# Performance work log

Measured on AMD Instinct MI355X. Metric: run time of the kernel, lower is better.

The kernel has to match this reference:

```python
import jax, jax.numpy as jnp
import numpy as np

N_NODES = 100000
N_EDGES = 1200000
D_FEAT = 64
THETA = (1.0, -0.8, 0.4, -0.1)  # polynomial coefficients, k = len(THETA)


def setup_inputs() -> dict:
    key = jax.random.key(0)
    k1, k2, k3 = jax.random.split(key, 3)
    feat = jax.random.normal(k1, (N_NODES, D_FEAT), dtype=jnp.float32)
    src = jax.random.randint(k2, (N_EDGES,), 0, N_NODES, dtype=jnp.int32)
    dst = jax.random.randint(k3, (N_EDGES,), 0, N_NODES, dtype=jnp.int32)
    return {"feat": feat, "src": src, "dst": dst}


def reference(feat, src, dst):
    # in-degrees: number of incoming edges per node (clamped to >= 1)
    deg = jax.ops.segment_sum(jnp.ones((N_EDGES,), feat.dtype), dst, num_segments=N_NODES)
    d_invsqrt = jnp.clip(deg, 1.0, None) ** -0.5  # [N]
    d = d_invsqrt[:, None]  # [N, 1]

    h = THETA[0] * feat
    for k in range(1, len(THETA)):
        # unnLaplacian: feat - D^{-1/2} A^T (D^{-1/2} feat)  (copy_u / sum over edges)
        msg = (feat * d)[src]                                   # [E, F] gather
        agg = jax.ops.segment_sum(msg, dst, num_segments=N_NODES)  # [N, F] scatter-add
        feat = feat - agg * d
        h = h + THETA[k] * feat
    return h
```

## Files before the change

kernel.cpp:

```cpp
#include <hip/hip_runtime.h>

#define D_FEAT 64
#define BSHIFT 8
#define MAXB 512
#define CHUNK 4096

typedef float nfloat4 __attribute__((ext_vector_type(4)));

__device__ inline unsigned short f2bf(float f) {
    unsigned u = __float_as_uint(f);
    unsigned r = u + 0x7fffu + ((u >> 16) & 1u);
    return (unsigned short)(r >> 16);
}
__device__ inline float bflo(unsigned w) { return __uint_as_float(w << 16); }
__device__ inline float bfhi(unsigned w) { return __uint_as_float(w & 0xffff0000u); }

__device__ inline void unpack8(uint4 u, float* v) {
    v[0] = bflo(u.x); v[1] = bfhi(u.x);
    v[2] = bflo(u.y); v[3] = bfhi(u.y);
    v[4] = bflo(u.z); v[5] = bfhi(u.z);
    v[6] = bflo(u.w); v[7] = bfhi(u.w);
}
__device__ inline uint4 pack8(const float* v) {
    uint4 u;
    u.x = (unsigned)f2bf(v[0]) | ((unsigned)f2bf(v[1]) << 16);
    u.y = (unsigned)f2bf(v[2]) | ((unsigned)f2bf(v[3]) << 16);
    u.z = (unsigned)f2bf(v[4]) | ((unsigned)f2bf(v[5]) << 16);
    u.w = (unsigned)f2bf(v[6]) | ((unsigned)f2bf(v[7]) << 16);
    return u;
}

__global__ void pre_kernel(const int* __restrict__ dst, int* __restrict__ bucket_tot,
                           const float4* __restrict__ f, uint4* __restrict__ fb,
                           int nE, int P, int nblk, int n8) {
    __shared__ int lh[MAXB];
    int b = blockIdx.x;
    if (b < nblk) {
        for (int i = threadIdx.x; i < P; i += blockDim.x) lh[i] = 0;
        __syncthreads();
        int s = b * CHUNK;
        int e1 = s + CHUNK; if (e1 > nE) e1 = nE;
        for (int e = s + threadIdx.x; e < e1; e += blockDim.x)
            atomicAdd(&lh[dst[e] >> BSHIFT], 1);
        __syncthreads();
        for (int i = threadIdx.x; i < P; i += blockDim.x) {
            int c = lh[i];
            if (c) atomicAdd(&bucket_tot[i], c);
        }
    } else {
        int i = (b - nblk) * 256 + threadIdx.x;
        if (i < n8) {
            float4 a = f[(size_t)i * 2];
            float4 c = f[(size_t)i * 2 + 1];
            float v[8] = {a.x, a.y, a.z, a.w, c.x, c.y, c.z, c.w};
            fb[i] = pack8(v);
        }
    }
}

__global__ void bscan_kernel(const int* __restrict__ bucket_tot, int* __restrict__ bucket_ptr,
                             int* __restrict__ cursor, int* __restrict__ row_ptr,
                             int P, int nE, int nN) {
    __shared__ int tmp[512];
    int tid = threadIdx.x;
    int v = (tid < P) ? bucket_tot[tid] : 0;
    tmp[tid] = v;
    __syncthreads();
    for (int off = 1; off < 512; off <<= 1) {
        int t2 = 0;
        if (tid >= off) t2 = tmp[tid - off];
        __syncthreads();
        tmp[tid] += t2;
        __syncthreads();
    }
    if (tid < P) {
        int start = tmp[tid] - v;
        bucket_ptr[tid] = start;
        cursor[tid] = start;
    }
    if (tid == 0) {
        bucket_ptr[P] = nE;
        row_ptr[nN] = nE;
    }
}

__global__ void scatter_part_kernel(const int* __restrict__ src, const int* __restrict__ dst,
                                    int* __restrict__ cursor, unsigned* __restrict__ part,
                                    int nE, int P) {
    __shared__ int cnt[MAXB];
    __shared__ int cur[MAXB];
    for (int i = threadIdx.x; i < P; i += blockDim.x) cnt[i] = 0;
    __syncthreads();
    int s = blockIdx.x * CHUNK;
    int e1 = s + CHUNK; if (e1 > nE) e1 = nE;
    int se[16], te[16];
#pragma unroll
    for (int k = 0; k < 16; ++k) {
        int e = s + k * 256 + threadIdx.x;
        if (e < e1) {
            se[k] = src[e];
            te[k] = dst[e];
            atomicAdd(&cnt[te[k] >> BSHIFT], 1);
        } else {
            te[k] = -1;
        }
    }
    __syncthreads();
    for (int i = threadIdx.x; i < P; i += blockDim.x) {
        int c = cnt[i];
        cur[i] = c ? atomicAdd(&cursor[i], c) : 0;
    }
    __syncthreads();
#pragma unroll
    for (int k = 0; k < 16; ++k) {
        if (te[k] >= 0) {
            int pos = atomicAdd(&cur[te[k] >> BSHIFT], 1);
            part[pos] = ((unsigned)se[k] << 8) | (unsigned)(te[k] & 255);
        }
    }
}

__global__ void bucket_csr_kernel(const unsigned* __restrict__ part,
                                  const int* __restrict__ bucket_ptr,
                                  int* __restrict__ row_ptr,
                                  float* __restrict__ dv, int* __restrict__ esrc, int nN) {
    __shared__ int hist[256];
    __shared__ int cur[256];
    __shared__ int scanT[256];
    int b = blockIdx.x;
    int tid = threadIdx.x;
    int bp0 = bucket_ptr[b], bp1 = bucket_ptr[b + 1];
    hist[tid] = 0;
    __syncthreads();
    for (int e = bp0 + tid; e < bp1; e += 256)
        atomicAdd(&hist[part[e] & 255u], 1);
    __syncthreads();
    int v = hist[tid];
    scanT[tid] = v;
    __syncthreads();
    for (int off = 1; off < 256; off <<= 1) {
        int t2 = 0;
        if (tid >= off) t2 = scanT[tid - off];
        __syncthreads();
        scanT[tid] += t2;
        __syncthreads();
    }
    int startv = scanT[tid] - v;
    cur[tid] = startv;
    int node = (b << BSHIFT) + tid;
    if (node < nN) {
        float fc = (float)(v < 1 ? 1 : v);
        dv[node] = rsqrtf(fc);
        row_ptr[node] = bp0 + startv;
    }
    __syncthreads();
    for (int e = bp0 + tid; e < bp1; e += 256) {
        unsigned p = part[e];
        int rank = atomicAdd(&cur[p & 255u], 1);
        esrc[bp0 + rank] = (int)(p >> 8);
    }
}

__global__ void poly_kernel(const uint4* __restrict__ fb_in, uint4* __restrict__ fb_out,
                            const int* __restrict__ row_ptr,
                            const int* __restrict__ esrc, const float* __restrict__ d,
                            const uint4* __restrict__ fb0, const uint4* __restrict__ fb1,
                            float* __restrict__ h, int final_step, int nN) {
    int wave = (blockIdx.x * blockDim.x + threadIdx.x) >> 6;
    int lane = threadIdx.x & 63;
    int sub  = lane >> 3;
    int q    = lane & 7;
    int t    = wave * 8 + sub;
    bool valid = (t < nN);
    if (!valid) t = nN - 1;

    int r0 = row_ptr[t], r1 = row_ptr[t + 1];
    if (!valid) r1 = r0;

    float acc[8];
#pragma unroll
    for (int c = 0; c < 8; ++c) acc[c] = 0.0f;

    int   sq = 0;
    float dq = 0.0f;
    if (r0 < r1) {
        int jc = r0 + q; if (jc > r1 - 1) jc = r1 - 1;
        sq = esrc[jc];
        dq = d[sq];
    }
    int j0 = r0;
    while (j0 < r1) {
        int jn = j0 + 8;
        int   sq_n = 0;
        float dq_n = 0.0f;
        if (jn < r1) {
            int jc = jn + q; if (jc > r1 - 1) jc = r1 - 1;
            sq_n = esrc[jc];
            dq_n = d[sq_n];
        }
        int m = r1 - j0; if (m > 8) m = 8;
#pragma unroll
        for (int u = 0; u < 4; ++u) {
            int bl = (sub << 3) + u;
            int   sb = __shfl(sq, bl, 64);
            float ds = __shfl(dq, bl, 64);
            ds = (u < m) ? ds : 0.0f;
            uint4 fv = fb_in[(size_t)sb * 8 + q];
            float v[8];
            unpack8(fv, v);
#pragma unroll
            for (int c = 0; c < 8; ++c) acc[c] = fmaf(v[c], ds, acc[c]);
        }
        if (m > 4) {
#pragma unroll
            for (int u = 4; u < 8; ++u) {
                int bl = (sub << 3) + u;
                int   sb = __shfl(sq, bl, 64);
                float ds = __shfl(dq, bl, 64);
                ds = (u < m) ? ds : 0.0f;
                uint4 fv = fb_in[(size_t)sb * 8 + q];
                float v[8];
                unpack8(fv, v);
#pragma unroll
                for (int c = 0; c < 8; ++c) acc[c] = fmaf(v[c], ds, acc[c]);
            }
        }
        sq = sq_n; dq = dq_n; j0 = jn;
    }

    if (!valid) return;
    size_t idx = (size_t)t * 8 + q;
    float dt = d[t];
    float fo[8];
    unpack8(fb_in[idx], fo);
    float fn[8];
#pragma unroll
    for (int c = 0; c < 8; ++c) fn[c] = fo[c] - acc[c] * dt;

    if (!final_step) {
        fb_out[idx] = pack8(fn);
    } else {
        float f1v[8];
        unpack8(fb1[idx], f1v);
        float f0v[8];
        unpack8(fb0[idx], f0v);
        float hv[8];
#pragma unroll
        for (int c = 0; c < 8; ++c)
            hv[c] = f0v[c] - 0.8f * f1v[c] + 0.4f * fo[c] - 0.1f * fn[c];
        nfloat4 h0 = {hv[0], hv[1], hv[2], hv[3]};
        nfloat4 h1 = {hv[4], hv[5], hv[6], hv[7]};
        nfloat4* hp = (nfloat4*)(h + (size_t)t * 64 + q * 8);
        __builtin_nontemporal_store(h0, hp);
        __builtin_nontemporal_store(h1, hp + 1);
    }
}

extern "C" void kernel_launch(void* const* d_in, const int* in_sizes, int n_in,
                              void* d_out, int out_size, void* d_ws, size_t ws_size,
                              hipStream_t stream) {
    const float* feat = (const float*)d_in[0];
    const int*   src  = (const int*)d_in[1];
    const int*   dst  = (const int*)d_in[2];
    float*       h    = (float*)d_out;

    const int nN = in_sizes[0] / D_FEAT;
    const int nE = in_sizes[1];

    const int P    = (nN + 255) >> 8;
    const int nblk = (nE + CHUNK - 1) / CHUNK;

    auto align = [](size_t x) { return (x + 255) & ~(size_t)255; };
    char* ws = (char*)d_ws;
    size_t off = 0;
    int*      bucket_tot = (int*)(ws + off);      off += align((size_t)P * 4);
    int*      bucket_ptr = (int*)(ws + off);      off += align((size_t)(P + 1) * 4);
    int*      cursor     = (int*)(ws + off);      off += align((size_t)P * 4);
    int*      row_ptr    = (int*)(ws + off);      off += align((size_t)(nN + 1) * 4);
    float*    dv         = (float*)(ws + off);    off += align((size_t)nN * 4);
    unsigned* part       = (unsigned*)(ws + off); off += align((size_t)nE * 4);
    int*      esrc       = (int*)(ws + off);      off += align((size_t)nE * 4);
    size_t fbBytes = (size_t)nN * D_FEAT * 2;
    uint4*    fb0        = (uint4*)(ws + off);    off += align(fbBytes);
    uint4*    fb1        = (uint4*)(ws + off);    off += align(fbBytes);
    uint4*    fb2;
    if (ws_size >= off + fbBytes) {
        fb2 = (uint4*)(ws + off);
    } else {
        fb2 = (uint4*)d_in[0];
    }

    const int n8 = nN * 8;
    const int tb = (n8 + 255) / 256;

    hipMemsetAsync(bucket_tot, 0, (size_t)P * 4, stream);
    pre_kernel         <<<nblk + tb, 256, 0, stream>>>(dst, bucket_tot, (const float4*)feat,
                                                       fb0, nE, P, nblk, n8);
    bscan_kernel       <<<1, 512, 0, stream>>>(bucket_tot, bucket_ptr, cursor, row_ptr,
                                               P, nE, nN);
    scatter_part_kernel<<<nblk, 256, 0, stream>>>(src, dst, cursor, part, nE, P);
    bucket_csr_kernel  <<<P, 256, 0, stream>>>(part, bucket_ptr, row_ptr, dv, esrc, nN);

    long long waves = ((long long)nN + 7) / 8;
    int polyBlocks = (int)((waves * 64 + 255) / 256);
    poly_kernel<<<polyBlocks, 256, 0, stream>>>(fb0, fb1, row_ptr, esrc, dv,
                                                nullptr, nullptr, nullptr, 0, nN);
    poly_kernel<<<polyBlocks, 256, 0, stream>>>(fb1, fb2, row_ptr, esrc, dv,
                                                nullptr, nullptr, nullptr, 0, nN);
    poly_kernel<<<polyBlocks, 256, 0, stream>>>(fb2, nullptr, row_ptr, esrc, dv,
                                                fb0, fb1, h, 1, nN);
}
```

Baseline: 209.8 us.

## Sort nodes by in-degree bins to balance work across poly_kernel wavefronts

Measured after the change: 225.3 us. +7.4%, slower.

```diff
diff --git a/kernel.cpp b/kernel.cpp
--- a/kernel.cpp
+++ b/kernel.cpp
@@ -4,6 +4,7 @@
 #define BSHIFT 8
 #define MAXB 512
 #define CHUNK 4096
+#define NBIN 64
 
 typedef float nfloat4 __attribute__((ext_vector_type(4)));
 
@@ -123,14 +124,17 @@
 __global__ void bucket_csr_kernel(const unsigned* __restrict__ part,
                                   const int* __restrict__ bucket_ptr,
                                   int* __restrict__ row_ptr,
-                                  float* __restrict__ dv, int* __restrict__ esrc, int nN) {
+                                  float* __restrict__ dv, int* __restrict__ esrc,
+                                  int* __restrict__ bin_tot, int nN) {
     __shared__ int hist[256];
     __shared__ int cur[256];
     __shared__ int scanT[256];
+    __shared__ int binh[NBIN];
     int b = blockIdx.x;
     int tid = threadIdx.x;
     int bp0 = bucket_ptr[b], bp1 = bucket_ptr[b + 1];
     hist[tid] = 0;
+    if (tid < NBIN) binh[tid] = 0;
     __syncthreads();
     for (int e = bp0 + tid; e < bp1; e += 256)
         atomicAdd(&hist[part[e] & 255u], 1);
@@ -152,8 +156,11 @@
         float fc = (float)(v < 1 ? 1 : v);
         dv[node] = rsqrtf(fc);
         row_ptr[node] = bp0 + startv;
-    }
-    __syncthreads();
+        int bin = v > (NBIN - 1) ? (NBIN - 1) : v;
+        atomicAdd(&binh[bin], 1);
+    }
+    __syncthreads();
+    if (tid < NBIN && binh[tid]) atomicAdd(&bin_tot[tid], binh[tid]);
     for (int e = bp0 + tid; e < bp1; e += 256) {
         unsigned p = part[e];
         int rank = atomicAdd(&cur[p & 255u], 1);
@@ -161,8 +168,45 @@
     }
 }
 
+__global__ void binscan_kernel(const int* __restrict__ bin_tot, int* __restrict__ bin_cur) {
+    int tid = threadIdx.x;
+    int v = bin_tot[tid];
+    int s = v;
+    for (int off = 1; off < 64; off <<= 1) {
+        int t2 = __shfl_up(s, off, 64);
+        if (tid >= off) s += t2;
+    }
+    bin_cur[tid] = s - v;
+}
+
+__global__ void perm_kernel(const int* __restrict__ row_ptr, int* __restrict__ bin_cur,
+                            int* __restrict__ perm, int nN) {
+    __shared__ int lcnt[NBIN];
+    __shared__ int lcur[NBIN];
+    int tid = threadIdx.x;
+    int t = blockIdx.x * 256 + tid;
+    if (tid < NBIN) lcnt[tid] = 0;
+    __syncthreads();
+    int bin = -1;
+    if (t < nN) {
+        int deg = row_ptr[t + 1] - row_ptr[t];
+        bin = deg > (NBIN - 1) ? (NBIN - 1) : deg;
+        atomicAdd(&lcnt[bin], 1);
+    }
+    __syncthreads();
+    if (tid < NBIN) {
+        int c = lcnt[tid];
+        lcur[tid] = c ? atomicAdd(&bin_cur[tid], c) : 0;
+    }
+    __syncthreads();
+    if (t < nN) {
+        int pos = atomicAdd(&lcur[bin], 1);
+        perm[pos] = t;
+    }
+}
+
 __global__ void poly_kernel(const uint4* __restrict__ fb_in, uint4* __restrict__ fb_out,
-                            const int* __restrict__ row_ptr,
+                            const int* __restrict__ row_ptr, const int* __restrict__ perm,
                             const int* __restrict__ esrc, const float* __restrict__ d,
                             const uint4* __restrict__ fb0, const uint4* __restrict__ fb1,
                             float* __restrict__ h, int final_step, int nN) {
@@ -170,9 +214,10 @@
     int lane = threadIdx.x & 63;
     int sub  = lane >> 3;
     int q    = lane & 7;
-    int t    = wave * 8 + sub;
-    bool valid = (t < nN);
-    if (!valid) t = nN - 1;
+    int i8   = wave * 8 + sub;
+    bool valid = (i8 < nN);
+    if (!valid) i8 = nN - 1;
+    int t = perm[i8];
 
     int r0 = row_ptr[t], r1 = row_ptr[t + 1];
     if (!valid) r1 = r0;
@@ -273,10 +318,13 @@
     auto align = [](size_t x) { return (x + 255) & ~(size_t)255; };
     char* ws = (char*)d_ws;
     size_t off = 0;
-    int*      bucket_tot = (int*)(ws + off);      off += align((size_t)P * 4);
+    int*      bucket_tot = (int*)(ws + off);      off += align((size_t)(P + NBIN) * 4);
+    int*      bin_tot    = bucket_tot + P;
     int*      bucket_ptr = (int*)(ws + off);      off += align((size_t)(P + 1) * 4);
     int*      cursor     = (int*)(ws + off);      off += align((size_t)P * 4);
+    int*      bin_cur    = (int*)(ws + off);      off += align((size_t)NBIN * 4);
     int*      row_ptr    = (int*)(ws + off);      off += align((size_t)(nN + 1) * 4);
+    int*      perm       = (int*)(ws + off);      off += align((size_t)nN * 4);
     float*    dv         = (float*)(ws + off);    off += align((size_t)nN * 4);
     unsigned* part       = (unsigned*)(ws + off); off += align((size_t)nE * 4);
     int*      esrc       = (int*)(ws + off);      off += align((size_t)nE * 4);
@@ -293,20 +341,23 @@
     const int n8 = nN * 8;
     const int tb = (n8 + 255) / 256;
 
-    hipMemsetAsync(bucket_tot, 0, (size_t)P * 4, stream);
+    hipMemsetAsync(bucket_tot, 0, (size_t)(P + NBIN) * 4, stream);
     pre_kernel         <<<nblk + tb, 256, 0, stream>>>(dst, bucket_tot, (const float4*)feat,
                                                        fb0, nE, P, nblk, n8);
     bscan_kernel       <<<1, 512, 0, stream>>>(bucket_tot, bucket_ptr, cursor, row_ptr,
                                                P, nE, nN);
     scatter_part_kernel<<<nblk, 256, 0, stream>>>(src, dst, cursor, part, nE, P);
-    bucket_csr_kernel  <<<P, 256, 0, stream>>>(part, bucket_ptr, row_ptr, dv, esrc, nN);
+    bucket_csr_kernel  <<<P, 256, 0, stream>>>(part, bucket_ptr, row_ptr, dv, esrc,
+                                               bin_tot, nN);
+    binscan_kernel     <<<1, 64, 0, stream>>>(bin_tot, bin_cur);
+    perm_kernel        <<<(nN + 255) / 256, 256, 0, stream>>>(row_ptr, bin_cur, perm, nN);
 
     long long waves = ((long long)nN + 7) / 8;
     int polyBlocks = (int)((waves * 64 + 255) / 256);
-    poly_kernel<<<polyBlocks, 256, 0, stream>>>(fb0, fb1, row_ptr, esrc, dv,
+    poly_kernel<<<polyBlocks, 256, 0, stream>>>(fb0, fb1, row_ptr, perm, esrc, dv,
                                                 nullptr, nullptr, nullptr, 0, nN);
-    poly_kernel<<<polyBlocks, 256, 0, stream>>>(fb1, fb2, row_ptr, esrc, dv,
+    poly_kernel<<<polyBlocks, 256, 0, stream>>>(fb1, fb2, row_ptr, perm, esrc, dv,
                                                 nullptr, nullptr, nullptr, 0, nN);
-    poly_kernel<<<polyBlocks, 256, 0, stream>>>(fb2, nullptr, row_ptr, esrc, dv,
+    poly_kernel<<<polyBlocks, 256, 0, stream>>>(fb2, nullptr, row_ptr, perm, esrc, dv,
                                                 fb0, fb1, h, 1, nN);
 }
```
